# Kernel tuning notes

Hardware: AMD Instinct MI355X
Metric: run time of the kernel (lower is better)

## Reference

```python
import jax, jax.numpy as jnp
import numpy as np

W_BIT = 4
A_BIT = 8
Q_GROUP_SIZE = 128  # weight quant group size along in_features


def _fake_quant_ste(t, n_bits, zero_point, q_group_size):
    """Per-group fake quant with straight-through estimator."""
    shape = t.shape
    if q_group_size > 0:
        q = t.reshape(-1, q_group_size)
    else:
        q = t.reshape(-1, shape[-1])
    if zero_point:
        max_val = jnp.max(q, axis=1, keepdims=True)
        min_val = jnp.min(q, axis=1, keepdims=True)
        max_int = 2 ** n_bits - 1
        min_int = 0
        scales = jnp.clip(max_val - min_val, 1e-5, None) / max_int
        zeros = jnp.clip(-jnp.round(min_val / scales), min_int, max_int)
    else:
        max_val = jnp.clip(jnp.max(jnp.abs(q), axis=1, keepdims=True), 1e-5, None)
        max_int = 2 ** (n_bits - 1) - 1
        min_int = -(2 ** (n_bits - 1))
        scales = max_val / max_int
        zeros = 0.0
    dq = (jnp.clip(jnp.round(q / scales) + zeros, min_int, max_int) - zeros) * scales
    dq = dq.reshape(shape)
    # STE: identity gradient through the quantizer
    return t + jax.lax.stop_gradient(dq - t)


def setup_inputs() -> dict:
    key = jax.random.key(0)
    k1, k2, k3, k4 = jax.random.split(key, 4)
    B, S, D_IN, D_OUT = 4, 2048, 4096, 4096
    x = jax.random.normal(k1, (B, S, D_IN), dtype=jnp.float32)
    weight = jax.random.normal(k2, (D_OUT, D_IN), dtype=jnp.float32) * 0.02
    bias = jax.random.normal(k3, (D_OUT,), dtype=jnp.float32) * 0.01
    log_scale = jax.random.normal(k4, (D_IN,), dtype=jnp.float32) * 0.1
    return {"x": x, "weight": weight, "bias": bias, "log_scale": log_scale}


def reference(x, weight, bias, log_scale):
    scale = jnp.clip(jnp.exp(log_scale), 1e-4, 1e4)  # [D_IN]
    x = x / scale                                    # broadcast over last dim
    weight = weight * scale[None, :]                 # [D_OUT, D_IN]
    # per-token (last-dim) symmetric activation quant
    xq = _fake_quant_ste(x, A_BIT, zero_point=False, q_group_size=-1)
    # per-group asymmetric weight quant
    wq = _fake_quant_ste(weight, W_BIT, zero_point=True, q_group_size=Q_GROUP_SIZE)
    # F.linear: x @ W^T + b
    return jnp.einsum("bsd,od->bso", xq, wq) + bias
```

## Files before the change

### kernel.cpp

```cpp
#include <hip/hip_runtime.h>
#include <hip/hip_bf16.h>
#include <cstdint>
#include <cstddef>

#define D_IN  4096
#define D_OUT 4096
#define M_TOK 8192
#define QG    128

typedef __bf16 bf16x8 __attribute__((ext_vector_type(8)));
typedef float  floatx4 __attribute__((ext_vector_type(4)));

__global__ __launch_bounds__(256) void scale_kernel(const float* __restrict__ ls,
                                                    float* __restrict__ scale,
                                                    float* __restrict__ rinv) {
    int i = blockIdx.x * 256 + threadIdx.x;
    if (i < D_IN) {
        float s = expf(ls[i]);
        s = fminf(fmaxf(s, 1e-4f), 1e4f);
        scale[i] = s;
        rinv[i]  = 1.0f / s;
    }
}

__global__ __launch_bounds__(256) void act_quant(const float* __restrict__ x,
                                                 const float* __restrict__ rinv,
                                                 __hip_bfloat16* __restrict__ xq) {
    const int row = blockIdx.x;
    const int tid = threadIdx.x;
    const float4* xr = (const float4*)(x + (size_t)row * D_IN);
    const float4* rv = (const float4*)rinv;

    float v[16];
    float amax = 0.f;
#pragma unroll
    for (int j = 0; j < 4; ++j) {
        int idx = j * 256 + tid;
        float4 xv = xr[idx];
        float4 ri = rv[idx];
        float a = xv.x * ri.x, b = xv.y * ri.y, c = xv.z * ri.z, d = xv.w * ri.w;
        v[j * 4 + 0] = a; v[j * 4 + 1] = b; v[j * 4 + 2] = c; v[j * 4 + 3] = d;
        amax = fmaxf(amax, fmaxf(fmaxf(fabsf(a), fabsf(b)), fmaxf(fabsf(c), fabsf(d))));
    }
#pragma unroll
    for (int off = 32; off > 0; off >>= 1)
        amax = fmaxf(amax, __shfl_xor(amax, off, 64));
    __shared__ float smax[4];
    if ((tid & 63) == 0) smax[tid >> 6] = amax;
    __syncthreads();
    float m = fmaxf(fmaxf(smax[0], smax[1]), fmaxf(smax[2], smax[3]));
    m = fmaxf(m, 1e-5f);
    const float s  = m / 127.0f;
    const float qs = 1.0f / s;

    ushort4* xo = (ushort4*)(xq + (size_t)row * D_IN);
#pragma unroll
    for (int j = 0; j < 4; ++j) {
        union { ushort4 u; __hip_bfloat16 h[4]; } p;
#pragma unroll
        for (int k = 0; k < 4; ++k) {
            float dq = fminf(fmaxf(rintf(v[j * 4 + k] * qs), -128.f), 127.f) * s;
            p.h[k] = __float2bfloat16(dq);
        }
        xo[j * 256 + tid] = p.u;
    }
}

__global__ __launch_bounds__(256) void w_quant(const float* __restrict__ wgt,
                                               const float* __restrict__ scale,
                                               __hip_bfloat16* __restrict__ wq) {
    const int wid  = blockIdx.x * 4 + (threadIdx.x >> 6);
    const int lane = threadIdx.x & 63;
    const size_t e0 = (size_t)wid * 256 + lane * 4;
    const int d0 = (int)(e0 & (D_IN - 1));

    float4 wv = *(const float4*)(wgt + e0);
    float4 sv = *(const float4*)(scale + d0);
    float w0 = wv.x * sv.x, w1 = wv.y * sv.y, w2 = wv.z * sv.z, w3 = wv.w * sv.w;

    float mx = fmaxf(fmaxf(w0, w1), fmaxf(w2, w3));
    float mn = fminf(fminf(w0, w1), fminf(w2, w3));
#pragma unroll
    for (int off = 16; off > 0; off >>= 1) {
        mx = fmaxf(mx, __shfl_xor(mx, off, 64));
        mn = fminf(mn, __shfl_xor(mn, off, 64));
    }
    const float s  = fmaxf(mx - mn, 1e-5f) / 15.0f;
    const float rs = 1.0f / s;
    const float z  = fminf(fmaxf(-rintf(mn * rs), 0.f), 15.f);

    union { ushort4 u; __hip_bfloat16 h[4]; } p;
    float wl[4] = {w0, w1, w2, w3};
#pragma unroll
    for (int k = 0; k < 4; ++k) {
        float dq = (fminf(fmaxf(rintf(wl[k] * rs) + z, 0.f), 15.f) - z) * s;
        p.h[k] = __float2bfloat16(dq);
    }
    *(ushort4*)(wq + e0) = p.u;
}

__global__ __launch_bounds__(256) void gemm_bt(const __hip_bfloat16* __restrict__ A,
                                               const __hip_bfloat16* __restrict__ B,
                                               const float* __restrict__ bias,
                                               float* __restrict__ C) {
    constexpr int K = D_IN;
    __shared__ unsigned short Alds[128 * 32];
    __shared__ unsigned short Blds[128 * 32];

    const int tid  = threadIdx.x;
    const int lane = tid & 63;
    const int w    = tid >> 6;
    const int bn   = blockIdx.x;
    const int bm   = blockIdx.y;
    const int wm   = (w >> 1) * 64;
    const int wn   = (w & 1) * 64;
    const int q    = lane >> 4;
    const int l16  = lane & 15;
    const int sw   = (l16 >> 1) & 3;
    const int colOff = ((q ^ sw)) * 8;

    floatx4 acc[4][4] = {};

    for (int k0 = 0; k0 < K; k0 += 32) {
        __syncthreads();
#pragma unroll
        for (int t = 0; t < 2; ++t) {
            int f = t * 256 + tid;
            int r = f >> 2;
            int c = (f & 3) ^ ((f >> 3) & 3);
            const __hip_bfloat16* ga = A + (size_t)(bm * 128 + r) * K + k0 + c * 8;
            __builtin_amdgcn_global_load_lds(
                (const __attribute__((address_space(1))) void*)ga,
                (__attribute__((address_space(3))) void*)(Alds + f * 8), 16, 0, 0);
            const __hip_bfloat16* gb = B + (size_t)(bn * 128 + r) * K + k0 + c * 8;
            __builtin_amdgcn_global_load_lds(
                (const __attribute__((address_space(1))) void*)gb,
                (__attribute__((address_space(3))) void*)(Blds + f * 8), 16, 0, 0);
        }
        __syncthreads();

        bf16x8 af[4], bfr[4];
#pragma unroll
        for (int i = 0; i < 4; ++i) {
            af[i]  = *(const bf16x8*)(Alds + (wm + i * 16 + l16) * 32 + colOff);
            bfr[i] = *(const bf16x8*)(Blds + (wn + i * 16 + l16) * 32 + colOff);
        }
#pragma unroll
        for (int mi = 0; mi < 4; ++mi)
#pragma unroll
            for (int ni = 0; ni < 4; ++ni)
                acc[mi][ni] = __builtin_amdgcn_mfma_f32_16x16x32_bf16(
                    af[mi], bfr[ni], acc[mi][ni], 0, 0, 0);
    }

    float bv[4];
#pragma unroll
    for (int ni = 0; ni < 4; ++ni)
        bv[ni] = bias[bn * 128 + wn + ni * 16 + l16];

#pragma unroll
    for (int mi = 0; mi < 4; ++mi) {
        int gm = bm * 128 + wm + mi * 16 + q * 4;
#pragma unroll
        for (int ni = 0; ni < 4; ++ni) {
            int gn = bn * 128 + wn + ni * 16 + l16;
            float* cp = C + (size_t)gm * D_OUT + gn;
#pragma unroll
            for (int r = 0; r < 4; ++r)
                cp[(size_t)r * D_OUT] = acc[mi][ni][r] + bv[ni];
        }
    }
}

extern "C" void kernel_launch(void* const* d_in, const int* in_sizes, int n_in,
                              void* d_out, int out_size, void* d_ws, size_t ws_size,
                              hipStream_t stream) {
    const float* x   = (const float*)d_in[0];
    const float* wgt = (const float*)d_in[1];
    const float* bia = (const float*)d_in[2];
    const float* ls  = (const float*)d_in[3];
    float* out = (float*)d_out;

    char* ws = (char*)d_ws;
    float*          scale = (float*)ws;
    float*          rinv  = (float*)(ws + (16 << 10));
    __hip_bfloat16* xq    = (__hip_bfloat16*)(ws + (64 << 10));
    __hip_bfloat16* wq    = (__hip_bfloat16*)(ws + (64 << 10) + ((size_t)64 << 20));

    scale_kernel<<<(D_IN + 255) / 256, 256, 0, stream>>>(ls, scale, rinv);
    act_quant<<<M_TOK, 256, 0, stream>>>(x, rinv, xq);
    w_quant<<<(D_OUT * D_IN / 256) / 4, 256, 0, stream>>>(wgt, scale, wq);

    dim3 grid(D_OUT / 128, M_TOK / 128);
    gemm_bt<<<grid, 256, 0, stream>>>(xq, wq, bia, out);
}
```

Baseline: 563.1 us.

## Rewrite GEMM with 256x256 tiles, 512 threads and double-buffered async LDS pipeline

The bf16 GEMM moves from 128x128 tiles with 4 waves and a load-sync-compute loop to 256x256 tiles with 8 waves. A-tiles and B-tiles are staged into double-buffered LDS with global_load_lds, prefetching two k-halves ahead under explicit vmcnt waits and barriers. Each wave issues its MFMAs at raised priority (s_setprio) between LDS fragment loads. This aims to hide global memory latency and raise arithmetic intensity, at the cost of 128 KB of LDS, high register pressure from a 32-accumulator tile, and fragile hand-written wait counts.

```diff
diff --git a/kernel.cpp b/kernel.cpp
--- a/kernel.cpp
+++ b/kernel.cpp
@@ -99,75 +99,166 @@
     *(ushort4*)(wq + e0) = p.u;
 }
 
-__global__ __launch_bounds__(256) void gemm_bt(const __hip_bfloat16* __restrict__ A,
-                                               const __hip_bfloat16* __restrict__ B,
-                                               const float* __restrict__ bias,
-                                               float* __restrict__ C) {
-    constexpr int K = D_IN;
-    __shared__ unsigned short Alds[128 * 32];
-    __shared__ unsigned short Blds[128 * 32];
+__global__ __launch_bounds__(512, 2) void gemm_bt(const __hip_bfloat16* __restrict__ A,
+                                                  const __hip_bfloat16* __restrict__ B,
+                                                  const float* __restrict__ bias,
+                                                  float* __restrict__ C) {
+    constexpr int K  = D_IN;
+    constexpr int NT = K / 64;
+    static_assert(NT >= 3, "pipeline needs >=3 tiles");
+    __shared__ __align__(16) unsigned short lds[2][2][2][256 * 32];
 
     const int tid  = threadIdx.x;
     const int lane = tid & 63;
     const int w    = tid >> 6;
+    const int wm   = w >> 2;
+    const int wn   = w & 3;
     const int bn   = blockIdx.x;
     const int bm   = blockIdx.y;
-    const int wm   = (w >> 1) * 64;
-    const int wn   = (w & 1) * 64;
     const int q    = lane >> 4;
     const int l16  = lane & 15;
-    const int sw   = (l16 >> 1) & 3;
-    const int colOff = ((q ^ sw)) * 8;
-
-    floatx4 acc[4][4] = {};
-
-    for (int k0 = 0; k0 < K; k0 += 32) {
-        __syncthreads();
-#pragma unroll
-        for (int t = 0; t < 2; ++t) {
-            int f = t * 256 + tid;
-            int r = f >> 2;
-            int c = (f & 3) ^ ((f >> 3) & 3);
-            const __hip_bfloat16* ga = A + (size_t)(bm * 128 + r) * K + k0 + c * 8;
-            __builtin_amdgcn_global_load_lds(
-                (const __attribute__((address_space(1))) void*)ga,
-                (__attribute__((address_space(3))) void*)(Alds + f * 8), 16, 0, 0);
-            const __hip_bfloat16* gb = B + (size_t)(bn * 128 + r) * K + k0 + c * 8;
-            __builtin_amdgcn_global_load_lds(
-                (const __attribute__((address_space(1))) void*)gb,
-                (__attribute__((address_space(3))) void*)(Blds + f * 8), 16, 0, 0);
-        }
-        __syncthreads();
-
-        bf16x8 af[4], bfr[4];
-#pragma unroll
-        for (int i = 0; i < 4; ++i) {
-            af[i]  = *(const bf16x8*)(Alds + (wm + i * 16 + l16) * 32 + colOff);
-            bfr[i] = *(const bf16x8*)(Blds + (wn + i * 16 + l16) * 32 + colOff);
-        }
-#pragma unroll
-        for (int mi = 0; mi < 4; ++mi)
-#pragma unroll
-            for (int ni = 0; ni < 4; ++ni)
-                acc[mi][ni] = __builtin_amdgcn_mfma_f32_16x16x32_bf16(
-                    af[mi], bfr[ni], acc[mi][ni], 0, 0, 0);
+    const int cOff = (q ^ ((l16 >> 1) & 3)) * 8;
+
+    const int g0 = tid, g1 = tid + 512;
+    const int r0 = g0 >> 2, c0 = (g0 & 3) ^ ((g0 >> 3) & 3);
+    const int r1 = g1 >> 2, c1 = (g1 & 3) ^ ((g1 >> 3) & 3);
+
+    const unsigned short* Au = (const unsigned short*)A;
+    const unsigned short* Bu = (const unsigned short*)B;
+    const unsigned short* sA0 = Au + (size_t)(bm * 256 + r0) * K + c0 * 8;
+    const unsigned short* sA1 = Au + (size_t)(bm * 256 + r1) * K + c1 * 8;
+    const unsigned short* sB0 = Bu + (size_t)(bn * 256 + r0) * K + c0 * 8;
+    const unsigned short* sB1 = Bu + (size_t)(bn * 256 + r1) * K + c1 * 8;
+
+    unsigned short* L    = &lds[0][0][0][0];
+    unsigned short* dst0 = L + (size_t)g0 * 8;
+    unsigned short* dst1 = L + (size_t)g1 * 8;
+
+    auto stage = [&](const unsigned short* s0, const unsigned short* s1, int regOff) {
+        __builtin_amdgcn_global_load_lds(
+            (const __attribute__((address_space(1))) void*)s0,
+            (__attribute__((address_space(3))) void*)(dst0 + regOff), 16, 0, 0);
+        __builtin_amdgcn_global_load_lds(
+            (const __attribute__((address_space(1))) void*)s1,
+            (__attribute__((address_space(3))) void*)(dst1 + regOff), 16, 0, 0);
+    };
+
+    stage(sA0,      sA1,      0);
+    stage(sB0,      sB1,      16384);
+    stage(sA0 + 32, sA1 + 32, 8192);
+    stage(sB0 + 32, sB1 + 32, 16384 + 8192);
+    stage(sA0 + 64, sA1 + 64, 32768);
+    stage(sB0 + 64, sB1 + 64, 32768 + 16384);
+    asm volatile("s_waitcnt vmcnt(8)" ::: "memory");
+    __builtin_amdgcn_sched_barrier(0);
+    __builtin_amdgcn_s_barrier();
+
+    floatx4 acc[8][4] = {};
+    const int rowA = wm * 128 + l16;
+    const int rowB = wn * 64  + l16;
+
+#pragma unroll 2
+    for (int t = 0; t < NT; ++t) {
+        const int buf  = (t & 1) * 32768;
+        const int bufN = buf ^ 32768;
+        const unsigned short* A0 = L + buf;
+        const unsigned short* A1 = L + buf + 8192;
+        const unsigned short* B0 = L + buf + 16384;
+        const unsigned short* B1 = L + buf + 16384 + 8192;
+        const bool s01    = (t + 1 < NT);
+        const bool s23    = (t + 2 < NT);
+        const bool steady = (t < NT - 2);
+        const int  k1 = (t + 1) * 64 + 32;
+        const int  k2 = (t + 2) * 64;
+
+        bf16x8 af[4], bf[4];
+
+#pragma unroll
+        for (int j = 0; j < 4; ++j) bf[j] = *(const bf16x8*)(B0 + (rowB + j * 16) * 32 + cOff);
+#pragma unroll
+        for (int i = 0; i < 4; ++i) af[i] = *(const bf16x8*)(A0 + (rowA + i * 16) * 32 + cOff);
+        if (s01) stage(sA0 + k1, sA1 + k1, bufN + 8192);
+        __builtin_amdgcn_s_barrier();
+        asm volatile("s_waitcnt lgkmcnt(0)" ::: "memory");
+        __builtin_amdgcn_sched_barrier(0);
+        __builtin_amdgcn_s_setprio(1);
+#pragma unroll
+        for (int i = 0; i < 4; ++i)
+#pragma unroll
+            for (int j = 0; j < 4; ++j)
+                acc[i][j] = __builtin_amdgcn_mfma_f32_16x16x32_bf16(af[i], bf[j], acc[i][j], 0, 0, 0);
+        __builtin_amdgcn_s_setprio(0);
+        __builtin_amdgcn_s_barrier();
+
+#pragma unroll
+        for (int i = 0; i < 4; ++i) af[i] = *(const bf16x8*)(A0 + (rowA + 64 + i * 16) * 32 + cOff);
+        if (s01) stage(sB0 + k1, sB1 + k1, bufN + 16384 + 8192);
+        __builtin_amdgcn_s_barrier();
+        asm volatile("s_waitcnt lgkmcnt(0)" ::: "memory");
+        __builtin_amdgcn_sched_barrier(0);
+        __builtin_amdgcn_s_setprio(1);
+#pragma unroll
+        for (int i = 0; i < 4; ++i)
+#pragma unroll
+            for (int j = 0; j < 4; ++j)
+                acc[4 + i][j] = __builtin_amdgcn_mfma_f32_16x16x32_bf16(af[i], bf[j], acc[4 + i][j], 0, 0, 0);
+        __builtin_amdgcn_s_setprio(0);
+        if (steady) { asm volatile("s_waitcnt vmcnt(8)" ::: "memory"); }
+        else        { asm volatile("s_waitcnt vmcnt(0)" ::: "memory"); }
+        __builtin_amdgcn_sched_barrier(0);
+        __builtin_amdgcn_s_barrier();
+
+#pragma unroll
+        for (int j = 0; j < 4; ++j) bf[j] = *(const bf16x8*)(B1 + (rowB + j * 16) * 32 + cOff);
+#pragma unroll
+        for (int i = 0; i < 4; ++i) af[i] = *(const bf16x8*)(A1 + (rowA + i * 16) * 32 + cOff);
+        if (s23) stage(sA0 + k2, sA1 + k2, buf);
+        __builtin_amdgcn_s_barrier();
+        asm volatile("s_waitcnt lgkmcnt(0)" ::: "memory");
+        __builtin_amdgcn_sched_barrier(0);
+        __builtin_amdgcn_s_setprio(1);
+#pragma unroll
+        for (int i = 0; i < 4; ++i)
+#pragma unroll
+            for (int j = 0; j < 4; ++j)
+                acc[i][j] = __builtin_amdgcn_mfma_f32_16x16x32_bf16(af[i], bf[j], acc[i][j], 0, 0, 0);
+        __builtin_amdgcn_s_setprio(0);
+        __builtin_amdgcn_s_barrier();
+
+#pragma unroll
+        for (int i = 0; i < 4; ++i) af[i] = *(const bf16x8*)(A1 + (rowA + 64 + i * 16) * 32 + cOff);
+        if (s23) stage(sB0 + k2, sB1 + k2, buf + 16384);
+        __builtin_amdgcn_s_barrier();
+        asm volatile("s_waitcnt lgkmcnt(0)" ::: "memory");
+        __builtin_amdgcn_sched_barrier(0);
+        __builtin_amdgcn_s_setprio(1);
+#pragma unroll
+        for (int i = 0; i < 4; ++i)
+#pragma unroll
+            for (int j = 0; j < 4; ++j)
+                acc[4 + i][j] = __builtin_amdgcn_mfma_f32_16x16x32_bf16(af[i], bf[j], acc[4 + i][j], 0, 0, 0);
+        __builtin_amdgcn_s_setprio(0);
+        if (steady) { asm volatile("s_waitcnt vmcnt(8)" ::: "memory"); }
+        else        { asm volatile("s_waitcnt vmcnt(0)" ::: "memory"); }
+        __builtin_amdgcn_sched_barrier(0);
+        __builtin_amdgcn_s_barrier();
     }
 
     float bv[4];
 #pragma unroll
-    for (int ni = 0; ni < 4; ++ni)
-        bv[ni] = bias[bn * 128 + wn + ni * 16 + l16];
-
-#pragma unroll
-    for (int mi = 0; mi < 4; ++mi) {
-        int gm = bm * 128 + wm + mi * 16 + q * 4;
-#pragma unroll
-        for (int ni = 0; ni < 4; ++ni) {
-            int gn = bn * 128 + wn + ni * 16 + l16;
+    for (int j = 0; j < 4; ++j)
+        bv[j] = bias[bn * 256 + wn * 64 + j * 16 + l16];
+
+#pragma unroll
+    for (int f = 0; f < 8; ++f) {
+        int gm = bm * 256 + wm * 128 + f * 16 + q * 4;
+#pragma unroll
+        for (int j = 0; j < 4; ++j) {
+            int gn = bn * 256 + wn * 64 + j * 16 + l16;
             float* cp = C + (size_t)gm * D_OUT + gn;
 #pragma unroll
             for (int r = 0; r < 4; ++r)
-                cp[(size_t)r * D_OUT] = acc[mi][ni][r] + bv[ni];
+                cp[(size_t)r * D_OUT] = acc[f][j][r] + bv[j];
         }
     }
 }
@@ -191,6 +282,6 @@
     act_quant<<<M_TOK, 256, 0, stream>>>(x, rinv, xq);
     w_quant<<<(D_OUT * D_IN / 256) / 4, 256, 0, stream>>>(wgt, scale, wq);
 
-    dim3 grid(D_OUT / 128, M_TOK / 128);
-    gemm_bt<<<grid, 256, 0, stream>>>(xq, wq, bia, out);
-}
+    dim3 grid(D_OUT / 256, M_TOK / 256);
+    gemm_bt<<<grid, 512, 0, stream>>>(xq, wq, bia, out);
+}
```

Result: faster. 516.6 us (-8.3%).
